# Kernel tuning notes

Hardware: AMD Instinct MI355X
Metric: run time of the kernel (lower is better)

The kernel has to match this reference:

```python
import jax, jax.numpy as jnp
import numpy as np

C_IN = 256
GROUP = C_IN // 4  # module hard-codes group = C_in/4 -> 4 channels per group
EPS = 1e-5

@jax.custom_vjp
def binarize(x):
    # 1-bit quantization: sign forward, hardtanh straight-through backward
    return jnp.sign(x)

def _bin_fwd(x):
    return jnp.sign(x), x

def _bin_bwd(x, g):
    return (g * (jnp.abs(x) <= 1.0).astype(g.dtype),)

binarize.defvjp(_bin_fwd, _bin_bwd)

def channel_shuffle(x, g):
    # [N,C,H,W] -> [N,g,C/g,H,W] -> [N,C/g,g,H,W] -> [N,C,H,W]
    N, C, H, W = x.shape
    return x.reshape(N, g, C // g, H, W).transpose(0, 2, 1, 3, 4).reshape(N, C, H, W)


def setup_inputs() -> dict:
    key = jax.random.key(0)
    ks = jax.random.split(key, 6)
    x = jax.random.normal(ks[0], (32, C_IN, 56, 56), jnp.float32)
    # grouped conv weight: [C_out, C_in/group, kH, kW] = [256, 4, 3, 3]
    weight = jax.random.normal(ks[1], (C_IN, C_IN // GROUP, 3, 3), jnp.float32) * 0.1
    gamma = 1.0 + 0.1 * jax.random.normal(ks[2], (C_IN,), jnp.float32)
    beta = 0.1 * jax.random.normal(ks[3], (C_IN,), jnp.float32)
    running_mean = 0.1 * jax.random.normal(ks[4], (C_IN,), jnp.float32)
    running_var = jax.random.uniform(ks[5], (C_IN,), jnp.float32, 0.5, 1.5)
    return dict(x=x, weight=weight, gamma=gamma, beta=beta,
                running_mean=running_mean, running_var=running_var)


def reference(x, weight, gamma, beta, running_mean, running_var):
    # BatchNorm2d (inference-mode, affine=True)
    inv = gamma * jax.lax.rsqrt(running_var + EPS)
    xb = x * inv[None, :, None, None] + (beta - running_mean * inv)[None, :, None, None]
    # Conv2d_1w1a: binarize activations and weights, grouped 3x3 conv, no bias
    a = binarize(xb)
    w = binarize(weight)
    out = jax.lax.conv_general_dilated(
        a, w,
        window_strides=(1, 1),
        padding=((1, 1), (1, 1)),
        dimension_numbers=('NCHW', 'OIHW', 'NCHW'),
        feature_group_count=GROUP,
    )
    out = channel_shuffle(out, GROUP)
    # stride == 1 -> shortcut is identity
    return out + x
```

## Files before the change

### kernel.cpp

```cpp
#include <hip/hip_runtime.h>
#include <stdint.h>

#define H 56
#define W 56
#define HW (H * W)
#define CIN 256
#define IMG (CIN * HW)
#define EPS 1e-5f

#define ROWW 8
#define TROWS 58
#define TILE_SZ (TROWS * ROWW)

__device__ __forceinline__ float mul_rn(float a, float b) {
    float d; asm("v_mul_f32 %0, %1, %2" : "=v"(d) : "v"(a), "v"(b)); return d;
}
__device__ __forceinline__ float add_rn(float a, float b) {
    float d; asm("v_add_f32 %0, %1, %2" : "=v"(d) : "v"(a), "v"(b)); return d;
}
__device__ __forceinline__ float sub_rn(float a, float b) {
    float d; asm("v_sub_f32 %0, %1, %2" : "=v"(d) : "v"(a), "v"(b)); return d;
}


__device__ __forceinline__ void stage_issue(const float* __restrict__ Xn, int g, int tid,
                                            float4 v[3][4]) {
#pragma unroll
    for (int i = 0; i < 3; ++i) {
        int t   = tid + i * 256;
        int r   = t / 14;
        int cg  = t - r * 14;
        int off = r * W + cg * 4;
#pragma unroll
        for (int ci = 0; ci < 4; ++ci)
            v[i][ci] = *reinterpret_cast<const float4*>(Xn + (size_t)(g * 4 + ci) * HW + off);
    }
}

__device__ __forceinline__ void bn_pack(const float4 q[4], const float inv[4], const float bias[4],
                                        uint32_t& s16, uint32_t& z16) {
    s16 = 0u; z16 = 0u;
#pragma unroll
    for (int ci = 0; ci < 4; ++ci) {
        float t0 = add_rn(mul_rn(q[ci].x, inv[ci]), bias[ci]);
        float t1 = add_rn(mul_rn(q[ci].y, inv[ci]), bias[ci]);
        float t2 = add_rn(mul_rn(q[ci].z, inv[ci]), bias[ci]);
        float t3 = add_rn(mul_rn(q[ci].w, inv[ci]), bias[ci]);
        s16 |= ((t0 > 0.f ? 1u : 0u) << ci)        | ((t1 > 0.f ? 1u : 0u) << (4 + ci))
             | ((t2 > 0.f ? 1u : 0u) << (8 + ci))  | ((t3 > 0.f ? 1u : 0u) << (12 + ci));
        z16 |= ((t0 != 0.f ? 1u : 0u) << ci)       | ((t1 != 0.f ? 1u : 0u) << (4 + ci))
             | ((t2 != 0.f ? 1u : 0u) << (8 + ci)) | ((t3 != 0.f ? 1u : 0u) << (12 + ci));
    }
}

__device__ __forceinline__ void stage_convert(const float4 v[3][4], const float inv[4],
                                              const float bias[4],
                                              uint32_t* s_t, uint32_t* z_t,
                                              int tid, const float* __restrict__ Xn, int g) {
#pragma unroll
    for (int i = 0; i < 3; ++i) {
        int t  = tid + i * 256;
        int r  = t / 14;
        int cg = t - r * 14;
        uint32_t s16, z16;
        bn_pack(v[i], inv, bias, s16, z16);
        reinterpret_cast<uint16_t*>(&s_t[(r + 1) * ROWW])[cg] = (uint16_t)s16;
        reinterpret_cast<uint16_t*>(&z_t[(r + 1) * ROWW])[cg] = (uint16_t)z16;
    }
    if (tid < 16) {
        int t   = 768 + tid;
        int r   = t / 14;
        int cg  = t - r * 14;
        int off = r * W + cg * 4;
        float4 q[4];
#pragma unroll
        for (int ci = 0; ci < 4; ++ci)
            q[ci] = *reinterpret_cast<const float4*>(Xn + (size_t)(g * 4 + ci) * HW + off);
        uint32_t s16, z16;
        bn_pack(q, inv, bias, s16, z16);
        reinterpret_cast<uint16_t*>(&s_t[(r + 1) * ROWW])[cg] = (uint16_t)s16;
        reinterpret_cast<uint16_t*>(&z_t[(r + 1) * ROWW])[cg] = (uint16_t)z16;
    }
}

__device__ __forceinline__ void phaseB(const uint32_t* s_t, const uint32_t* z_t,
                                       const float* __restrict__ Xn, float* __restrict__ On,
                                       int g, int tid,
                                       const uint32_t wsj[4][3], const uint32_t wzj[4][3],
                                       bool full) {
    for (int task = tid; task < 56 * 14; task += 256) {
        int h  = task / 14;
        int cg = task - h * 14;
        int w0 = cg * 4;
        size_t pbase = (size_t)h * W + w0;

        float4 sc[4];
#pragma unroll
        for (int j = 0; j < 4; ++j)
            sc[j] = *reinterpret_cast<const float4*>(Xn + (size_t)(j * 64 + g) * HW + pbase);

        uint64_t vs[3], vz[3];
        int off;
        if (w0 == 0) {
            off = 0;
#pragma unroll
            for (int r = 0; r < 3; ++r) {
                int base = (h + r) * ROWW;
                vs[r] = (((uint64_t)s_t[base] | ((uint64_t)s_t[base + 1] << 32)) << 4);
                vz[r] = (((uint64_t)z_t[base] | ((uint64_t)z_t[base + 1] << 32)) << 4);
            }
        } else {
            int st = 4 * w0 - 4;
            int i0 = st >> 5;
            off = st & 31;
#pragma unroll
            for (int r = 0; r < 3; ++r) {
                int base = (h + r) * ROWW + i0;
                vs[r] = ((uint64_t)s_t[base] | ((uint64_t)s_t[base + 1] << 32));
                vz[r] = ((uint64_t)z_t[base] | ((uint64_t)z_t[base + 1] << 32));
            }
        }

        int res[4][4];
        if (full) {
#pragma unroll
            for (int k = 0; k < 4; ++k) {
                int sh = off + 4 * k;
                uint32_t s0 = (uint32_t)(vs[0] >> sh) & 0xFFFu;
                uint32_t s1 = (uint32_t)(vs[1] >> sh) & 0xFFFu;
                uint32_t s2 = (uint32_t)(vs[2] >> sh) & 0xFFFu;
                uint32_t z0 = (uint32_t)(vz[0] >> sh) & 0xFFFu;
                uint32_t z1 = (uint32_t)(vz[1] >> sh) & 0xFFFu;
                uint32_t z2 = (uint32_t)(vz[2] >> sh) & 0xFFFu;
                int vb = __popc(z0) + __popc(z1) + __popc(z2);
#pragma unroll
                for (int j = 0; j < 4; ++j) {
                    int pc = __popc((s0 ^ wsj[j][0]) & z0)
                           + __popc((s1 ^ wsj[j][1]) & z1)
                           + __popc((s2 ^ wsj[j][2]) & z2);
                    res[j][k] = vb - 2 * pc;
                }
            }
        } else {
#pragma unroll
            for (int k = 0; k < 4; ++k) {
                int sh = off + 4 * k;
                uint32_t s0 = (uint32_t)(vs[0] >> sh) & 0xFFFu;
                uint32_t s1 = (uint32_t)(vs[1] >> sh) & 0xFFFu;
                uint32_t s2 = (uint32_t)(vs[2] >> sh) & 0xFFFu;
                uint32_t z0 = (uint32_t)(vz[0] >> sh) & 0xFFFu;
                uint32_t z1 = (uint32_t)(vz[1] >> sh) & 0xFFFu;
                uint32_t z2 = (uint32_t)(vz[2] >> sh) & 0xFFFu;
#pragma unroll
                for (int j = 0; j < 4; ++j) {
                    uint32_t m0 = z0 & wzj[j][0];
                    uint32_t m1 = z1 & wzj[j][1];
                    uint32_t m2 = z2 & wzj[j][2];
                    int vb = __popc(m0) + __popc(m1) + __popc(m2);
                    int pc = __popc((s0 ^ wsj[j][0]) & m0)
                           + __popc((s1 ^ wsj[j][1]) & m1)
                           + __popc((s2 ^ wsj[j][2]) & m2);
                    res[j][k] = vb - 2 * pc;
                }
            }
        }

#pragma unroll
        for (int j = 0; j < 4; ++j) {
            size_t cofs = (size_t)(j * 64 + g) * HW + pbase;
            float4 o;
            o.x = add_rn((float)res[j][0], sc[j].x);
            o.y = add_rn((float)res[j][1], sc[j].y);
            o.z = add_rn((float)res[j][2], sc[j].z);
            o.w = add_rn((float)res[j][3], sc[j].w);
            *reinterpret_cast<float4*>(On + cofs) = o;
        }
    }
}

__global__ __launch_bounds__(256, 4)
void binconv_kernel(const float* __restrict__ X,
                    const float* __restrict__ Wt,
                    const float* __restrict__ gamma,
                    const float* __restrict__ beta,
                    const float* __restrict__ mean,
                    const float* __restrict__ var,
                    float* __restrict__ out, int nHalf) {
    __shared__ uint32_t s_tile[2][TILE_SZ];
    __shared__ uint32_t z_tile[2][TILE_SZ];
    __shared__ uint32_t ws_l[4][3];
    __shared__ uint32_t wz_l[4][3];

    const int bx  = blockIdx.x;
    const int n0  = bx >> 6;
    const int g   = bx & 63;
    const int tid = threadIdx.x;

    for (int i = tid; i < 2 * TILE_SZ; i += 256) {
        (&s_tile[0][0])[i] = 0u;
        (&z_tile[0][0])[i] = 0u;
    }

    if (tid < 4) {
        const float* wc = Wt + (size_t)(g * 4 + tid) * 36;
        for (int r = 0; r < 3; ++r) {
            uint32_t s = 0, z = 0;
            for (int ci = 0; ci < 4; ++ci)
                for (int kw = 0; kw < 3; ++kw) {
                    float v = wc[ci * 9 + r * 3 + kw];
                    int b = kw * 4 + ci;
                    s |= (v > 0.f  ? 1u : 0u) << b;
                    z |= (v != 0.f ? 1u : 0u) << b;
                }
            ws_l[tid][r] = s; wz_l[tid][r] = z;
        }
    }

    float inv[4], bias[4];
#pragma unroll
    for (int ci = 0; ci < 4; ++ci) {
        int c = g * 4 + ci;
        float s  = sqrtf(var[c] + EPS);
        float r  = 1.0f / s;
        float iv = mul_rn(gamma[c], r);
        inv[ci]  = iv;
        bias[ci] = sub_rn(beta[c], mul_rn(mean[c], iv));
    }

    const float* Xn0 = X   + (size_t)n0 * IMG;
    const float* Xn1 = X   + (size_t)(n0 + nHalf) * IMG;
    float*       On0 = out + (size_t)n0 * IMG;
    float*       On1 = out + (size_t)(n0 + nHalf) * IMG;

    float4 v0[3][4];
    stage_issue(Xn0, g, tid, v0);

    __syncthreads();

    stage_convert(v0, inv, bias, s_tile[0], z_tile[0], tid, Xn0, g);

    uint32_t wsj[4][3], wzj[4][3];
    bool full = true;
#pragma unroll
    for (int j = 0; j < 4; ++j)
#pragma unroll
        for (int r = 0; r < 3; ++r) {
            wsj[j][r] = __builtin_amdgcn_readfirstlane(ws_l[j][r]);
            wzj[j][r] = __builtin_amdgcn_readfirstlane(wz_l[j][r]);
            full = full && (wzj[j][r] == 0xFFFu);
        }

    __syncthreads();

    float4 v1[3][4];
    stage_issue(Xn1, g, tid, v1);

    phaseB(s_tile[0], z_tile[0], Xn0, On0, g, tid, wsj, wzj, full);

    stage_convert(v1, inv, bias, s_tile[1], z_tile[1], tid, Xn1, g);

    __syncthreads();

    phaseB(s_tile[1], z_tile[1], Xn1, On1, g, tid, wsj, wzj, full);
}

extern "C" void kernel_launch(void* const* d_in, const int* in_sizes, int n_in,
                              void* d_out, int out_size, void* d_ws, size_t ws_size,
                              hipStream_t stream) {
    const float* X     = (const float*)d_in[0];
    const float* Wt    = (const float*)d_in[1];
    const float* gamma = (const float*)d_in[2];
    const float* beta  = (const float*)d_in[3];
    const float* mean  = (const float*)d_in[4];
    const float* var   = (const float*)d_in[5];
    float* out = (float*)d_out;

    int N     = in_sizes[0] / IMG;
    int nHalf = N >> 1;

    binconv_kernel<<<nHalf * 64, 256, 0, stream>>>(X, Wt, gamma, beta, mean, var, out, nHalf);
}
```

Baseline: 198.7 us.

## Split each image-group into two half-height blocks with halo rows and raise occupancy

Each block now handles half of the 56 rows (28 output rows plus a 1-row halo, 29 input rows) for one group, which doubles the grid size and shrinks the shared-memory tiles. The launch bound rises from 4 to 8 blocks per unit, and the BN scale/bias are moved into scalar registers via readfirstlane so the multiplies use scalar operands. The second image's loads are interleaved with the first image's compute using sched_barriers. In exchange, each block reloads two halo rows, adding some redundant global traffic, and register pressure is tighter.

```diff
diff --git a/kernel.cpp b/kernel.cpp
--- a/kernel.cpp
+++ b/kernel.cpp
@@ -9,8 +9,10 @@
 #define EPS 1e-5f
 
 #define ROWW 8
-#define TROWS 58
-#define TILE_SZ (TROWS * ROWW)
+#define TR2 30
+#define TSZ (TR2 * ROWW)
+#define ATASKS 406
+#define BTASKS 392
 
 __device__ __forceinline__ float mul_rn(float a, float b) {
     float d; asm("v_mul_f32 %0, %1, %2" : "=v"(d) : "v"(a), "v"(b)); return d;
@@ -21,31 +23,39 @@
 __device__ __forceinline__ float sub_rn(float a, float b) {
     float d; asm("v_sub_f32 %0, %1, %2" : "=v"(d) : "v"(a), "v"(b)); return d;
 }
-
-
-__device__ __forceinline__ void stage_issue(const float* __restrict__ Xn, int g, int tid,
-                                            float4 v[3][4]) {
-#pragma unroll
-    for (int i = 0; i < 3; ++i) {
-        int t   = tid + i * 256;
-        int r   = t / 14;
-        int cg  = t - r * 14;
-        int off = r * W + cg * 4;
-#pragma unroll
-        for (int ci = 0; ci < 4; ++ci)
-            v[i][ci] = *reinterpret_cast<const float4*>(Xn + (size_t)(g * 4 + ci) * HW + off);
-    }
-}
-
-__device__ __forceinline__ void bn_pack(const float4 q[4], const float inv[4], const float bias[4],
+__device__ __forceinline__ float mul_rn_sv(float s, float v) {
+    float d; asm("v_mul_f32 %0, %1, %2" : "=v"(d) : "s"(s), "v"(v)); return d;
+}
+__device__ __forceinline__ float add_rn_sv(float s, float v) {
+    float d; asm("v_add_f32 %0, %1, %2" : "=v"(d) : "s"(s), "v"(v)); return d;
+}
+__device__ __forceinline__ float rfl_f(float x) {
+    return __int_as_float(__builtin_amdgcn_readfirstlane(__float_as_int(x)));
+}
+
+
+struct Stage { float4 q[4]; };
+
+__device__ __forceinline__ void issueA(const float* __restrict__ Xn, int g, int half,
+                                       int t, Stage& st) {
+    int ar = t / 14;
+    int cg = t - ar * 14;
+    int ir = ar + half * 27;
+    const float* base = Xn + (size_t)(g * 4) * HW + ir * W + cg * 4;
+#pragma unroll
+    for (int ci = 0; ci < 4; ++ci)
+        st.q[ci] = *reinterpret_cast<const float4*>(base + (size_t)ci * HW);
+}
+
+__device__ __forceinline__ void bn_pack(const Stage& st, const float inv[4], const float bias[4],
                                         uint32_t& s16, uint32_t& z16) {
     s16 = 0u; z16 = 0u;
 #pragma unroll
     for (int ci = 0; ci < 4; ++ci) {
-        float t0 = add_rn(mul_rn(q[ci].x, inv[ci]), bias[ci]);
-        float t1 = add_rn(mul_rn(q[ci].y, inv[ci]), bias[ci]);
-        float t2 = add_rn(mul_rn(q[ci].z, inv[ci]), bias[ci]);
-        float t3 = add_rn(mul_rn(q[ci].w, inv[ci]), bias[ci]);
+        float t0 = add_rn_sv(bias[ci], mul_rn_sv(inv[ci], st.q[ci].x));
+        float t1 = add_rn_sv(bias[ci], mul_rn_sv(inv[ci], st.q[ci].y));
+        float t2 = add_rn_sv(bias[ci], mul_rn_sv(inv[ci], st.q[ci].z));
+        float t3 = add_rn_sv(bias[ci], mul_rn_sv(inv[ci], st.q[ci].w));
         s16 |= ((t0 > 0.f ? 1u : 0u) << ci)        | ((t1 > 0.f ? 1u : 0u) << (4 + ci))
              | ((t2 > 0.f ? 1u : 0u) << (8 + ci))  | ((t3 > 0.f ? 1u : 0u) << (12 + ci));
         z16 |= ((t0 != 0.f ? 1u : 0u) << ci)       | ((t1 != 0.f ? 1u : 0u) << (4 + ci))
@@ -53,132 +63,110 @@
     }
 }
 
-__device__ __forceinline__ void stage_convert(const float4 v[3][4], const float inv[4],
-                                              const float bias[4],
-                                              uint32_t* s_t, uint32_t* z_t,
-                                              int tid, const float* __restrict__ Xn, int g) {
-#pragma unroll
-    for (int i = 0; i < 3; ++i) {
-        int t  = tid + i * 256;
-        int r  = t / 14;
-        int cg = t - r * 14;
-        uint32_t s16, z16;
-        bn_pack(v[i], inv, bias, s16, z16);
-        reinterpret_cast<uint16_t*>(&s_t[(r + 1) * ROWW])[cg] = (uint16_t)s16;
-        reinterpret_cast<uint16_t*>(&z_t[(r + 1) * ROWW])[cg] = (uint16_t)z16;
-    }
-    if (tid < 16) {
-        int t   = 768 + tid;
-        int r   = t / 14;
-        int cg  = t - r * 14;
-        int off = r * W + cg * 4;
-        float4 q[4];
-#pragma unroll
-        for (int ci = 0; ci < 4; ++ci)
-            q[ci] = *reinterpret_cast<const float4*>(Xn + (size_t)(g * 4 + ci) * HW + off);
-        uint32_t s16, z16;
-        bn_pack(q, inv, bias, s16, z16);
-        reinterpret_cast<uint16_t*>(&s_t[(r + 1) * ROWW])[cg] = (uint16_t)s16;
-        reinterpret_cast<uint16_t*>(&z_t[(r + 1) * ROWW])[cg] = (uint16_t)z16;
-    }
-}
-
-__device__ __forceinline__ void phaseB(const uint32_t* s_t, const uint32_t* z_t,
-                                       const float* __restrict__ Xn, float* __restrict__ On,
-                                       int g, int tid,
-                                       const uint32_t wsj[4][3], const uint32_t wzj[4][3],
-                                       bool full) {
-    for (int task = tid; task < 56 * 14; task += 256) {
-        int h  = task / 14;
-        int cg = task - h * 14;
-        int w0 = cg * 4;
-        size_t pbase = (size_t)h * W + w0;
-
-        float4 sc[4];
-#pragma unroll
-        for (int j = 0; j < 4; ++j)
-            sc[j] = *reinterpret_cast<const float4*>(Xn + (size_t)(j * 64 + g) * HW + pbase);
-
-        uint64_t vs[3], vz[3];
-        int off;
-        if (w0 == 0) {
-            off = 0;
-#pragma unroll
-            for (int r = 0; r < 3; ++r) {
-                int base = (h + r) * ROWW;
-                vs[r] = (((uint64_t)s_t[base] | ((uint64_t)s_t[base + 1] << 32)) << 4);
-                vz[r] = (((uint64_t)z_t[base] | ((uint64_t)z_t[base + 1] << 32)) << 4);
+__device__ __forceinline__ void convA(const Stage& st, const float inv[4], const float bias[4],
+                                      uint32_t* s_t, uint32_t* z_t, int t, int half) {
+    int ar = t / 14;
+    int cg = t - ar * 14;
+    int rt = ar + 1 - half;
+    uint32_t s16, z16;
+    bn_pack(st, inv, bias, s16, z16);
+    reinterpret_cast<uint16_t*>(&s_t[rt * ROWW])[cg] = (uint16_t)s16;
+    reinterpret_cast<uint16_t*>(&z_t[rt * ROWW])[cg] = (uint16_t)z16;
+}
+
+__device__ __forceinline__ void taskB(const uint32_t* s_t, const uint32_t* z_t,
+                                      const float* __restrict__ Xn, float* __restrict__ On,
+                                      int g, int half, int task,
+                                      const uint32_t wsj[4][3], const uint32_t wzj[4][3],
+                                      bool full) {
+    int hl = task / 14;
+    int cg = task - hl * 14;
+    int w0 = cg * 4;
+
+    uint64_t vs[3], vz[3];
+    int off;
+    if (w0 == 0) {
+        off = 0;
+#pragma unroll
+        for (int r = 0; r < 3; ++r) {
+            int base = (hl + r) * ROWW;
+            vs[r] = (((uint64_t)s_t[base] | ((uint64_t)s_t[base + 1] << 32)) << 4);
+            vz[r] = (((uint64_t)z_t[base] | ((uint64_t)z_t[base + 1] << 32)) << 4);
+        }
+    } else {
+        int st = 4 * w0 - 4;
+        int i0 = st >> 5;
+        off = st & 31;
+#pragma unroll
+        for (int r = 0; r < 3; ++r) {
+            int base = (hl + r) * ROWW + i0;
+            vs[r] = ((uint64_t)s_t[base] | ((uint64_t)s_t[base + 1] << 32));
+            vz[r] = ((uint64_t)z_t[base] | ((uint64_t)z_t[base + 1] << 32));
+        }
+    }
+
+    int res[4][4];
+    if (full) {
+#pragma unroll
+        for (int k = 0; k < 4; ++k) {
+            int sh = off + 4 * k;
+            uint32_t s0 = (uint32_t)(vs[0] >> sh) & 0xFFFu;
+            uint32_t s1 = (uint32_t)(vs[1] >> sh) & 0xFFFu;
+            uint32_t s2 = (uint32_t)(vs[2] >> sh) & 0xFFFu;
+            uint32_t z0 = (uint32_t)(vz[0] >> sh) & 0xFFFu;
+            uint32_t z1 = (uint32_t)(vz[1] >> sh) & 0xFFFu;
+            uint32_t z2 = (uint32_t)(vz[2] >> sh) & 0xFFFu;
+            int vb = __popc(z0) + __popc(z1) + __popc(z2);
+#pragma unroll
+            for (int j = 0; j < 4; ++j) {
+                int pc = __popc((s0 ^ wsj[j][0]) & z0)
+                       + __popc((s1 ^ wsj[j][1]) & z1)
+                       + __popc((s2 ^ wsj[j][2]) & z2);
+                res[j][k] = vb - 2 * pc;
             }
-        } else {
-            int st = 4 * w0 - 4;
-            int i0 = st >> 5;
-            off = st & 31;
-#pragma unroll
-            for (int r = 0; r < 3; ++r) {
-                int base = (h + r) * ROWW + i0;
-                vs[r] = ((uint64_t)s_t[base] | ((uint64_t)s_t[base + 1] << 32));
-                vz[r] = ((uint64_t)z_t[base] | ((uint64_t)z_t[base + 1] << 32));
+        }
+    } else {
+#pragma unroll
+        for (int k = 0; k < 4; ++k) {
+            int sh = off + 4 * k;
+            uint32_t s0 = (uint32_t)(vs[0] >> sh) & 0xFFFu;
+            uint32_t s1 = (uint32_t)(vs[1] >> sh) & 0xFFFu;
+            uint32_t s2 = (uint32_t)(vs[2] >> sh) & 0xFFFu;
+            uint32_t z0 = (uint32_t)(vz[0] >> sh) & 0xFFFu;
+            uint32_t z1 = (uint32_t)(vz[1] >> sh) & 0xFFFu;
+            uint32_t z2 = (uint32_t)(vz[2] >> sh) & 0xFFFu;
+#pragma unroll
+            for (int j = 0; j < 4; ++j) {
+                uint32_t m0 = z0 & wzj[j][0];
+                uint32_t m1 = z1 & wzj[j][1];
+                uint32_t m2 = z2 & wzj[j][2];
+                int vb = __popc(m0) + __popc(m1) + __popc(m2);
+                int pc = __popc((s0 ^ wsj[j][0]) & m0)
+                       + __popc((s1 ^ wsj[j][1]) & m1)
+                       + __popc((s2 ^ wsj[j][2]) & m2);
+                res[j][k] = vb - 2 * pc;
             }
         }
-
-        int res[4][4];
-        if (full) {
-#pragma unroll
-            for (int k = 0; k < 4; ++k) {
-                int sh = off + 4 * k;
-                uint32_t s0 = (uint32_t)(vs[0] >> sh) & 0xFFFu;
-                uint32_t s1 = (uint32_t)(vs[1] >> sh) & 0xFFFu;
-                uint32_t s2 = (uint32_t)(vs[2] >> sh) & 0xFFFu;
-                uint32_t z0 = (uint32_t)(vz[0] >> sh) & 0xFFFu;
-                uint32_t z1 = (uint32_t)(vz[1] >> sh) & 0xFFFu;
-                uint32_t z2 = (uint32_t)(vz[2] >> sh) & 0xFFFu;
-                int vb = __popc(z0) + __popc(z1) + __popc(z2);
-#pragma unroll
-                for (int j = 0; j < 4; ++j) {
-                    int pc = __popc((s0 ^ wsj[j][0]) & z0)
-                           + __popc((s1 ^ wsj[j][1]) & z1)
-                           + __popc((s2 ^ wsj[j][2]) & z2);
-                    res[j][k] = vb - 2 * pc;
-                }
-            }
-        } else {
-#pragma unroll
-            for (int k = 0; k < 4; ++k) {
-                int sh = off + 4 * k;
-                uint32_t s0 = (uint32_t)(vs[0] >> sh) & 0xFFFu;
-                uint32_t s1 = (uint32_t)(vs[1] >> sh) & 0xFFFu;
-                uint32_t s2 = (uint32_t)(vs[2] >> sh) & 0xFFFu;
-                uint32_t z0 = (uint32_t)(vz[0] >> sh) & 0xFFFu;
-                uint32_t z1 = (uint32_t)(vz[1] >> sh) & 0xFFFu;
-                uint32_t z2 = (uint32_t)(vz[2] >> sh) & 0xFFFu;
-#pragma unroll
-                for (int j = 0; j < 4; ++j) {
-                    uint32_t m0 = z0 & wzj[j][0];
-                    uint32_t m1 = z1 & wzj[j][1];
-                    uint32_t m2 = z2 & wzj[j][2];
-                    int vb = __popc(m0) + __popc(m1) + __popc(m2);
-                    int pc = __popc((s0 ^ wsj[j][0]) & m0)
-                           + __popc((s1 ^ wsj[j][1]) & m1)
-                           + __popc((s2 ^ wsj[j][2]) & m2);
-                    res[j][k] = vb - 2 * pc;
-                }
-            }
-        }
-
-#pragma unroll
-        for (int j = 0; j < 4; ++j) {
-            size_t cofs = (size_t)(j * 64 + g) * HW + pbase;
-            float4 o;
-            o.x = add_rn((float)res[j][0], sc[j].x);
-            o.y = add_rn((float)res[j][1], sc[j].y);
-            o.z = add_rn((float)res[j][2], sc[j].z);
-            o.w = add_rn((float)res[j][3], sc[j].w);
-            *reinterpret_cast<float4*>(On + cofs) = o;
-        }
-    }
-}
-
-__global__ __launch_bounds__(256, 4)
+    }
+
+    size_t pbase = (size_t)(half * 28 + hl) * W + w0;
+    float4 sc[4];
+#pragma unroll
+    for (int j = 0; j < 4; ++j)
+        sc[j] = *reinterpret_cast<const float4*>(Xn + (size_t)(j * 64 + g) * HW + pbase);
+#pragma unroll
+    for (int j = 0; j < 4; ++j) {
+        size_t cofs = (size_t)(j * 64 + g) * HW + pbase;
+        float4 o;
+        o.x = add_rn((float)res[j][0], sc[j].x);
+        o.y = add_rn((float)res[j][1], sc[j].y);
+        o.z = add_rn((float)res[j][2], sc[j].z);
+        o.w = add_rn((float)res[j][3], sc[j].w);
+        *reinterpret_cast<float4*>(On + cofs) = o;
+    }
+}
+
+__global__ __launch_bounds__(256, 8)
 void binconv_kernel(const float* __restrict__ X,
                     const float* __restrict__ Wt,
                     const float* __restrict__ gamma,
@@ -186,20 +174,30 @@
                     const float* __restrict__ mean,
                     const float* __restrict__ var,
                     float* __restrict__ out, int nHalf) {
-    __shared__ uint32_t s_tile[2][TILE_SZ];
-    __shared__ uint32_t z_tile[2][TILE_SZ];
+    __shared__ uint32_t s_tile[2][TSZ];
+    __shared__ uint32_t z_tile[2][TSZ];
     __shared__ uint32_t ws_l[4][3];
     __shared__ uint32_t wz_l[4][3];
 
-    const int bx  = blockIdx.x;
-    const int n0  = bx >> 6;
-    const int g   = bx & 63;
-    const int tid = threadIdx.x;
-
-    for (int i = tid; i < 2 * TILE_SZ; i += 256) {
+    const int bx   = blockIdx.x;
+    const int half = bx & 1;
+    const int g    = (bx >> 1) & 63;
+    const int n0   = bx >> 7;
+    const int tid  = threadIdx.x;
+
+    for (int i = tid; i < 2 * TSZ; i += 256) {
         (&s_tile[0][0])[i] = 0u;
         (&z_tile[0][0])[i] = 0u;
     }
+
+    const float* Xn0 = X   + (size_t)n0 * IMG;
+    const float* Xn1 = X   + (size_t)(n0 + nHalf) * IMG;
+    float*       On0 = out + (size_t)n0 * IMG;
+    float*       On1 = out + (size_t)(n0 + nHalf) * IMG;
+
+    Stage a0, a1;
+    issueA(Xn0, g, half, tid, a0);
+    if (tid < ATASKS - 256) issueA(Xn0, g, half, tid + 256, a1);
 
     if (tid < 4) {
         const float* wc = Wt + (size_t)(g * 4 + tid) * 36;
@@ -223,21 +221,14 @@
         float s  = sqrtf(var[c] + EPS);
         float r  = 1.0f / s;
         float iv = mul_rn(gamma[c], r);
-        inv[ci]  = iv;
-        bias[ci] = sub_rn(beta[c], mul_rn(mean[c], iv));
-    }
-
-    const float* Xn0 = X   + (size_t)n0 * IMG;
-    const float* Xn1 = X   + (size_t)(n0 + nHalf) * IMG;
-    float*       On0 = out + (size_t)n0 * IMG;
-    float*       On1 = out + (size_t)(n0 + nHalf) * IMG;
-
-    float4 v0[3][4];
-    stage_issue(Xn0, g, tid, v0);
+        inv[ci]  = rfl_f(iv);
+        bias[ci] = rfl_f(sub_rn(beta[c], mul_rn(mean[c], iv)));
+    }
 
     __syncthreads();
 
-    stage_convert(v0, inv, bias, s_tile[0], z_tile[0], tid, Xn0, g);
+    convA(a0, inv, bias, s_tile[0], z_tile[0], tid, half);
+    if (tid < ATASKS - 256) convA(a1, inv, bias, s_tile[0], z_tile[0], tid + 256, half);
 
     uint32_t wsj[4][3], wzj[4][3];
     bool full = true;
@@ -252,16 +243,25 @@
 
     __syncthreads();
 
-    float4 v1[3][4];
-    stage_issue(Xn1, g, tid, v1);
-
-    phaseB(s_tile[0], z_tile[0], Xn0, On0, g, tid, wsj, wzj, full);
-
-    stage_convert(v1, inv, bias, s_tile[1], z_tile[1], tid, Xn1, g);
+    issueA(Xn1, g, half, tid, a0);
+    __builtin_amdgcn_sched_barrier(0);
+
+    taskB(s_tile[0], z_tile[0], Xn0, On0, g, half, tid, wsj, wzj, full);
+
+    convA(a0, inv, bias, s_tile[1], z_tile[1], tid, half);
+    if (tid < ATASKS - 256) issueA(Xn1, g, half, tid + 256, a1);
+    __builtin_amdgcn_sched_barrier(0);
+
+    if (tid < BTASKS - 256)
+        taskB(s_tile[0], z_tile[0], Xn0, On0, g, half, tid + 256, wsj, wzj, full);
+
+    if (tid < ATASKS - 256) convA(a1, inv, bias, s_tile[1], z_tile[1], tid + 256, half);
 
     __syncthreads();
 
-    phaseB(s_tile[1], z_tile[1], Xn1, On1, g, tid, wsj, wzj, full);
+    taskB(s_tile[1], z_tile[1], Xn1, On1, g, half, tid, wsj, wzj, full);
+    if (tid < BTASKS - 256)
+        taskB(s_tile[1], z_tile[1], Xn1, On1, g, half, tid + 256, wsj, wzj, full);
 }
 
 extern "C" void kernel_launch(void* const* d_in, const int* in_sizes, int n_in,
@@ -278,5 +278,5 @@
     int N     = in_sizes[0] / IMG;
     int nHalf = N >> 1;
 
-    binconv_kernel<<<nHalf * 64, 256, 0, stream>>>(X, Wt, gamma, beta, mean, var, out, nHalf);
-}
+    binconv_kernel<<<nHalf * 64 * 2, 256, 0, stream>>>(X, Wt, gamma, beta, mean, var, out, nHalf);
+}
```

New measurement: 220.9 us. +11.2%, slower.
